# Optimization experiments

Measured on AMD Instinct MI355X. Metric: run time of the kernel, lower is better.

The kernel has to match this reference:

```python
import jax, jax.numpy as jnp
import numpy as np

MAX_NUM_LEVELS = 3.5
NUM_LEVELS = 4  # mip levels 0..3 (levels clamped to [0, 2.5])


def affine_grid(matrix, N, H, W):
    # F.affine_grid, align_corners=False. matrix: (N,2,3) -> grid (N,H,W,2) in xy order.
    xs = (jnp.arange(W, dtype=jnp.float32) + 0.5) * (2.0 / W) - 1.0
    ys = (jnp.arange(H, dtype=jnp.float32) + 0.5) * (2.0 / H) - 1.0
    gy, gx = jnp.meshgrid(ys, xs, indexing='ij')
    base = jnp.stack([gx, gy, jnp.ones_like(gx)], axis=-1)  # (H,W,3)
    return jnp.einsum('hwk,nik->nhwi', base, matrix)  # (N,H,W,2)


def grid_sample_border(img, grid):
    # bilinear grid_sample, padding_mode='border', align_corners=False
    N, C, H, W = img.shape
    x = (grid[..., 0] + 1.0) * (W / 2.0) - 0.5
    y = (grid[..., 1] + 1.0) * (H / 2.0) - 0.5
    x0 = jnp.floor(x); y0 = jnp.floor(y)
    tx = x - x0; ty = y - y0
    x0i = jnp.clip(x0.astype(jnp.int32), 0, W - 1)
    x1i = jnp.clip(x0.astype(jnp.int32) + 1, 0, W - 1)
    y0i = jnp.clip(y0.astype(jnp.int32), 0, H - 1)
    y1i = jnp.clip(y0.astype(jnp.int32) + 1, 0, H - 1)
    b = jnp.arange(N)[:, None, None]
    g = lambda yi, xi: img[b, :, yi, xi]  # (N,Ho,Wo,C) gather
    out = (g(y0i, x0i) * ((1 - tx) * (1 - ty))[..., None]
           + g(y0i, x1i) * (tx * (1 - ty))[..., None]
           + g(y1i, x0i) * ((1 - tx) * ty)[..., None]
           + g(y1i, x1i) * (tx * ty)[..., None])
    return jnp.transpose(out, (0, 3, 1, 2))  # (N,C,Ho,Wo)


def blur_downsample(x):
    N, C, H, W = x.shape
    k1 = jnp.array([1., 3., 3., 1.], dtype=x.dtype) / 8.0
    k = k1[:, None] * k1[None, :]
    xp = jnp.pad(x, ((0, 0), (0, 0), (1, 2), (1, 2)), mode='reflect')
    kernel = jnp.broadcast_to(k[None, None], (C, 1, 4, 4))
    return jax.lax.conv_general_dilated(xp, kernel, window_strides=(2, 2), padding='VALID',
                                        feature_group_count=C,
                                        dimension_numbers=('NCHW', 'OIHW', 'NCHW'))


def compute_levels(grid, H, W):
    # per-pixel mip LOD from local stretch of the sampling grid (in source pixel units)
    coords = (grid + 1.0) * 0.5 * jnp.array([W, H], dtype=grid.dtype)  # (N,Ho,Wo,2)
    dx = coords[:, :-1, 1:] - coords[:, :-1, :-1]
    dy = coords[:, 1:, :-1] - coords[:, :-1, :-1]
    scale = jnp.maximum(jnp.linalg.norm(dx, axis=-1), jnp.linalg.norm(dy, axis=-1))
    scale = jnp.pad(scale, ((0, 0), (0, 1), (0, 1)), mode='edge')  # (N,Ho,Wo)
    levels = jnp.log2(jnp.maximum(scale, 1.0))
    return jnp.clip(levels, 0.0, MAX_NUM_LEVELS - 1.0)


def mipmap_warp(img, grid):
    N, C, H, W = img.shape
    levels = compute_levels(grid, H, W)  # (N,Ho,Wo)
    pyr = [img]
    for _ in range(NUM_LEVELS - 1):
        pyr.append(blur_downsample(pyr[-1]))
    samples = jnp.stack([grid_sample_border(p, grid) for p in pyr], axis=0)  # (L,N,C,Ho,Wo)
    ls = jnp.arange(NUM_LEVELS, dtype=levels.dtype)[:, None, None, None]
    w = jnp.clip(1.0 - jnp.abs(levels[None] - ls), 0.0, 1.0)  # trilinear blend weights (L,N,Ho,Wo)
    return jnp.einsum('lnhw,lnchw->nchw', w, samples)


def setup_inputs() -> dict:
    key = jax.random.key(0)
    k1, k2, k3 = jax.random.split(key, 3)
    N, C, H, W, D = 64, 3, 256, 256, 512
    img = jax.random.normal(k1, (N, C, H, W), dtype=jnp.float32)
    features = jax.random.normal(k2, (N, D), dtype=jnp.float32)
    # learned head params (zero-init in torch; small random here so the warp is nontrivial)
    lin_w = jax.random.normal(k3, (4, D), dtype=jnp.float32) * 0.02
    lin_b = jnp.zeros((4,), dtype=jnp.float32)
    return {'img': img, 'features': features, 'lin_w': lin_w, 'lin_b': lin_b}


def reference(img, features, lin_w, lin_b):
    params = features @ lin_w.T + lin_b  # (N,4)
    rot = jnp.tanh(params[:, 0:1]) * jnp.pi
    scale = jnp.exp(params[:, 1:2])
    sx, sy = params[:, 2:3], params[:, 3:4]
    c, s = jnp.cos(rot), jnp.sin(rot)
    matrix = jnp.concatenate([scale * c, -scale * s, sx, scale * s, scale * c, sy], axis=1).reshape(-1, 2, 3)
    affine_params = jnp.concatenate([rot, scale, sx, sy], axis=1)
    N, C, H, W = img.shape
    grid = affine_grid(matrix, N, H, W)
    out = mipmap_warp(img, grid)
    return out, grid, matrix, affine_params
```

## Files before the change

kernel.cpp:

```cpp
#include <hip/hip_runtime.h>
#include <math.h>

#define N_B 64
#define C_CH 3
#define H_IMG 256
#define W_IMG 256
#define D_FEAT 512

#define OUT_OFF_GRID   12582912
#define OUT_OFF_MATRIX 20971520
#define OUT_OFF_AFFINE 20971904

__global__ void params_kernel(const float* __restrict__ features,
                              const float* __restrict__ lin_w,
                              const float* __restrict__ lin_b,
                              float* __restrict__ out_matrix,
                              float* __restrict__ out_affine,
                              float* __restrict__ ws_params)
{
    const int n = blockIdx.x;
    const int t = threadIdx.x;
    const float* f = features + n * D_FEAT;
    float f0 = f[t];
    float f1 = f[t + 256];
    float a0 = f0 * lin_w[0 * D_FEAT + t] + f1 * lin_w[0 * D_FEAT + t + 256];
    float a1 = f0 * lin_w[1 * D_FEAT + t] + f1 * lin_w[1 * D_FEAT + t + 256];
    float a2 = f0 * lin_w[2 * D_FEAT + t] + f1 * lin_w[2 * D_FEAT + t + 256];
    float a3 = f0 * lin_w[3 * D_FEAT + t] + f1 * lin_w[3 * D_FEAT + t + 256];

    __shared__ float red[4][256];
    red[0][t] = a0; red[1][t] = a1; red[2][t] = a2; red[3][t] = a3;
    __syncthreads();
    for (int s = 128; s > 0; s >>= 1) {
        if (t < s) {
            red[0][t] += red[0][t + s];
            red[1][t] += red[1][t + s];
            red[2][t] += red[2][t + s];
            red[3][t] += red[3][t + s];
        }
        __syncthreads();
    }
    if (t == 0) {
        float p0 = red[0][0] + lin_b[0];
        float p1 = red[1][0] + lin_b[1];
        float p2 = red[2][0] + lin_b[2];
        float p3 = red[3][0] + lin_b[3];
        float rot   = tanhf(p0) * 3.14159265358979323846f;
        float scale = expf(p1);
        float c = cosf(rot), s = sinf(rot);
        float m00 = scale * c, m01 = -scale * s, m02 = p2;
        float m10 = scale * s, m11 =  scale * c, m12 = p3;
        out_matrix[n * 6 + 0] = m00;
        out_matrix[n * 6 + 1] = m01;
        out_matrix[n * 6 + 2] = m02;
        out_matrix[n * 6 + 3] = m10;
        out_matrix[n * 6 + 4] = m11;
        out_matrix[n * 6 + 5] = m12;
        out_affine[n * 4 + 0] = rot;
        out_affine[n * 4 + 1] = scale;
        out_affine[n * 4 + 2] = p2;
        out_affine[n * 4 + 3] = p3;
        float lv = log2f(fmaxf(scale, 1.0f));
        lv = fminf(fmaxf(lv, 0.0f), 2.5f);
        ws_params[n * 8 + 0] = m00;
        ws_params[n * 8 + 1] = m01;
        ws_params[n * 8 + 2] = m02;
        ws_params[n * 8 + 3] = m10;
        ws_params[n * 8 + 4] = m11;
        ws_params[n * 8 + 5] = m12;
        ws_params[n * 8 + 6] = lv;
        ws_params[n * 8 + 7] = 0.0f;
    }
}

template<int Hs, int Ws>
__global__ void down_kernel(const float* __restrict__ src, float* __restrict__ dst)
{
    constexpr int Hd = Hs / 2, Wd = Ws / 2;
    constexpr int PAIRS = Wd / 2;

    const int idx = blockIdx.x * blockDim.x + threadIdx.x;
    const int t   = idx & (PAIRS - 1);
    const int i   = (idx / PAIRS) & (Hd - 1);
    const int nc  = idx / (PAIRS * Hd);

    const float* __restrict__ s = src + (size_t)nc * Hs * Ws;

    int r[4];
#pragma unroll
    for (int a = 0; a < 4; a++) {
        int q = 2 * i + a - 1;
        if (q < 0) q = -q;
        if (q >= Hs) q = 2 * Hs - 2 - q;
        r[a] = q;
    }
    const int c4 = 4 * t;
    const int li = (t > 0)         ? c4 - 1 : 1;
    const int ri = (t < PAIRS - 1) ? c4 + 4 : Ws - 2;

    const float k0 = 0.125f, k1 = 0.375f;
    const float kr[4] = {0.125f, 0.375f, 0.375f, 0.125f};

    float acc0 = 0.0f, acc1 = 0.0f;
#pragma unroll
    for (int a = 0; a < 4; a++) {
        const float* row = s + (size_t)r[a] * Ws;
        float4 v = *(const float4*)(row + c4);
        float L = row[li];
        float R = row[ri];
        float h0 = k0 * L   + k1 * v.x + k1 * v.y + k0 * v.z;
        float h1 = k0 * v.y + k1 * v.z + k1 * v.w + k0 * R;
        acc0 += kr[a] * h0;
        acc1 += kr[a] * h1;
    }
    float2* d2 = (float2*)(dst + (size_t)nc * Hd * Wd + (size_t)i * Wd);
    d2[t] = make_float2(acc0, acc1);
}

__device__ __forceinline__ void sample_level(const float* __restrict__ p, int n, int l,
                                             float X, float Y, float out[3])
{
    const int Wl = W_IMG >> l;
    const int Hl = H_IMG >> l;
    float x = (X + 1.0f) * (0.5f * (float)Wl) - 0.5f;
    float y = (Y + 1.0f) * (0.5f * (float)Hl) - 0.5f;
    float x0f = floorf(x), y0f = floorf(y);
    float tx = x - x0f, ty = y - y0f;
    int x0 = (int)x0f, y0 = (int)y0f;
    int x0i = min(max(x0,     0), Wl - 1);
    int x1i = min(max(x0 + 1, 0), Wl - 1);
    int y0i = min(max(y0,     0), Hl - 1);
    int y1i = min(max(y0 + 1, 0), Hl - 1);
    float w00 = (1.0f - tx) * (1.0f - ty);
    float w01 = tx * (1.0f - ty);
    float w10 = (1.0f - tx) * ty;
    float w11 = tx * ty;
    const float* base = p + (size_t)n * C_CH * Hl * Wl;
#pragma unroll
    for (int c = 0; c < C_CH; c++) {
        const float* pc = base + (size_t)c * Hl * Wl;
        out[c] = w00 * pc[y0i * Wl + x0i] + w01 * pc[y0i * Wl + x1i]
               + w10 * pc[y1i * Wl + x0i] + w11 * pc[y1i * Wl + x1i];
    }
}

__device__ __forceinline__ const float* lvl_ptr(int l, const float* img,
                                                const float* p1, const float* p2,
                                                const float* p3)
{
    return (l == 0) ? img : ((l == 1) ? p1 : ((l == 2) ? p2 : p3));
}

__global__ void warp_kernel(const float* __restrict__ img,
                            const float* __restrict__ pyr1,
                            const float* __restrict__ pyr2,
                            const float* __restrict__ pyr3,
                            const float* __restrict__ ws_params,
                            float* __restrict__ out,
                            float* __restrict__ gridOut)
{
    const int n = blockIdx.y;
    const int tile = blockIdx.x;
    const int w = ((tile & 7) << 5) + (threadIdx.x & 31);
    const int h = ((tile >> 3) << 3) + (threadIdx.x >> 5);

    const float* P = ws_params + n * 8;
    float m00 = P[0], m01 = P[1], m02 = P[2];
    float m10 = P[3], m11 = P[4], m12 = P[5];
    float lv  = P[6];

    float gx = ((float)w + 0.5f) * (2.0f / (float)W_IMG) - 1.0f;
    float gy = ((float)h + 0.5f) * (2.0f / (float)H_IMG) - 1.0f;
    float X = m00 * gx + m01 * gy + m02;
    float Y = m10 * gx + m11 * gy + m12;

    float2* g2 = (float2*)gridOut;
    g2[(size_t)(n * H_IMG + h) * W_IMG + w] = make_float2(X, Y);

    int   l0   = (int)lv;
    float frac = lv - (float)l0;

    float c0[3];
    sample_level(lvl_ptr(l0, img, pyr1, pyr2, pyr3), n, l0, X, Y, c0);

    float r0, r1, r2;
    if (frac > 0.0f) {
        float c1[3];
        sample_level(lvl_ptr(l0 + 1, img, pyr1, pyr2, pyr3), n, l0 + 1, X, Y, c1);
        float w0 = 1.0f - frac;
        r0 = w0 * c0[0] + frac * c1[0];
        r1 = w0 * c0[1] + frac * c1[1];
        r2 = w0 * c0[2] + frac * c1[2];
    } else {
        r0 = c0[0]; r1 = c0[1]; r2 = c0[2];
    }

    size_t base = ((size_t)(n * C_CH + 0) * H_IMG + h) * W_IMG + w;
    out[base]                             = r0;
    out[base + (size_t)H_IMG * W_IMG]     = r1;
    out[base + (size_t)2 * H_IMG * W_IMG] = r2;
}

extern "C" void kernel_launch(void* const* d_in, const int* in_sizes, int n_in,
                              void* d_out, int out_size, void* d_ws, size_t ws_size,
                              hipStream_t stream)
{
    const float* img      = (const float*)d_in[0];
    const float* features = (const float*)d_in[1];
    const float* lin_w    = (const float*)d_in[2];
    const float* lin_b    = (const float*)d_in[3];

    float* out        = (float*)d_out;
    float* gridOut    = out + OUT_OFF_GRID;
    float* out_matrix = out + OUT_OFF_MATRIX;
    float* out_affine = out + OUT_OFF_AFFINE;

    float* ws        = (float*)d_ws;
    float* ws_params = ws;
    float* pyr1 = ws + 1024;
    float* pyr2 = pyr1 + (size_t)N_B * C_CH * 128 * 128;
    float* pyr3 = pyr2 + (size_t)N_B * C_CH * 64 * 64;

    params_kernel<<<N_B, 256, 0, stream>>>(features, lin_w, lin_b,
                                           out_matrix, out_affine, ws_params);

    int t1 = N_B * C_CH * 128 * 64;
    down_kernel<256, 256><<<t1 / 256, 256, 0, stream>>>(img,  pyr1);
    int t2 = N_B * C_CH * 64 * 32;
    down_kernel<128, 128><<<t2 / 256, 256, 0, stream>>>(pyr1, pyr2);
    int t3 = N_B * C_CH * 32 * 16;
    down_kernel<64, 64><<<t3 / 256, 256, 0, stream>>>(pyr2, pyr3);

    warp_kernel<<<dim3(H_IMG * W_IMG / 256, N_B), 256, 0, stream>>>(
        img, pyr1, pyr2, pyr3, ws_params, out, gridOut);
}
```

Before: 198.4 us.

## Widen downsample per-thread output, pair bilinear loads, retile warp, nontemporal stores

The downsample kernel now produces four outputs per thread from two float4 loads, which halves the thread count and widens its stores. Bilinear sampling fetches each horizontal texel pair with a single float2 load, using selects to handle the clamped edges. The warp kernel remaps threads to 16x4 sub-tiles for better 2D gather locality, and writes grid and output with nontemporal stores. The float2 loads may be misaligned when xp is odd, and the new tiling makes the output stores less contiguous.

```diff
diff --git a/kernel.cpp b/kernel.cpp
--- a/kernel.cpp
+++ b/kernel.cpp
@@ -77,12 +77,12 @@
 __global__ void down_kernel(const float* __restrict__ src, float* __restrict__ dst)
 {
     constexpr int Hd = Hs / 2, Wd = Ws / 2;
-    constexpr int PAIRS = Wd / 2;
+    constexpr int QUADS = Wd / 4;
 
     const int idx = blockIdx.x * blockDim.x + threadIdx.x;
-    const int t   = idx & (PAIRS - 1);
-    const int i   = (idx / PAIRS) & (Hd - 1);
-    const int nc  = idx / (PAIRS * Hd);
+    const int t   = idx & (QUADS - 1);
+    const int i   = (idx / QUADS) & (Hd - 1);
+    const int nc  = idx / (QUADS * Hd);
 
     const float* __restrict__ s = src + (size_t)nc * Hs * Ws;
 
@@ -94,31 +94,43 @@
         if (q >= Hs) q = 2 * Hs - 2 - q;
         r[a] = q;
     }
-    const int c4 = 4 * t;
-    const int li = (t > 0)         ? c4 - 1 : 1;
-    const int ri = (t < PAIRS - 1) ? c4 + 4 : Ws - 2;
+    const int c8 = 8 * t;
+    const int li = (t > 0)         ? c8 - 1 : 1;
+    const int ri = (t < QUADS - 1) ? c8 + 8 : Ws - 2;
 
     const float k0 = 0.125f, k1 = 0.375f;
     const float kr[4] = {0.125f, 0.375f, 0.375f, 0.125f};
 
-    float acc0 = 0.0f, acc1 = 0.0f;
+    float acc0 = 0.f, acc1 = 0.f, acc2 = 0.f, acc3 = 0.f;
 #pragma unroll
     for (int a = 0; a < 4; a++) {
         const float* row = s + (size_t)r[a] * Ws;
-        float4 v = *(const float4*)(row + c4);
+        float4 A = *(const float4*)(row + c8);
+        float4 B = *(const float4*)(row + c8 + 4);
         float L = row[li];
         float R = row[ri];
-        float h0 = k0 * L   + k1 * v.x + k1 * v.y + k0 * v.z;
-        float h1 = k0 * v.y + k1 * v.z + k1 * v.w + k0 * R;
+        float h0 = k0 * L   + k1 * A.x + k1 * A.y + k0 * A.z;
+        float h1 = k0 * A.y + k1 * A.z + k1 * A.w + k0 * B.x;
+        float h2 = k0 * A.w + k1 * B.x + k1 * B.y + k0 * B.z;
+        float h3 = k0 * B.y + k1 * B.z + k1 * B.w + k0 * R;
         acc0 += kr[a] * h0;
         acc1 += kr[a] * h1;
-    }
-    float2* d2 = (float2*)(dst + (size_t)nc * Hd * Wd + (size_t)i * Wd);
-    d2[t] = make_float2(acc0, acc1);
-}
-
-__device__ __forceinline__ void sample_level(const float* __restrict__ p, int n, int l,
-                                             float X, float Y, float out[3])
+        acc2 += kr[a] * h2;
+        acc3 += kr[a] * h3;
+    }
+    float4* d4 = (float4*)(dst + (size_t)nc * Hd * Wd + (size_t)i * Wd + 4 * t);
+    *d4 = make_float4(acc0, acc1, acc2, acc3);
+}
+
+__device__ __forceinline__ const float* lvl_ptr(int l, const float* img,
+                                                const float* p1, const float* p2,
+                                                const float* p3)
+{
+    return (l == 0) ? img : ((l == 1) ? p1 : ((l == 2) ? p2 : p3));
+}
+
+__device__ __forceinline__ void sample_level_pair(const float* __restrict__ p, int n, int l,
+                                                  float X, float Y, float out[3])
 {
     const int Wl = W_IMG >> l;
     const int Hl = H_IMG >> l;
@@ -127,10 +139,11 @@
     float x0f = floorf(x), y0f = floorf(y);
     float tx = x - x0f, ty = y - y0f;
     int x0 = (int)x0f, y0 = (int)y0f;
-    int x0i = min(max(x0,     0), Wl - 1);
-    int x1i = min(max(x0 + 1, 0), Wl - 1);
     int y0i = min(max(y0,     0), Hl - 1);
     int y1i = min(max(y0 + 1, 0), Hl - 1);
+    int xp = min(max(x0, 0), Wl - 2);
+    const bool selHi0 = (x0 >= Wl - 1);
+    const bool selLo1 = (x0 < 0);
     float w00 = (1.0f - tx) * (1.0f - ty);
     float w01 = tx * (1.0f - ty);
     float w10 = (1.0f - tx) * ty;
@@ -139,16 +152,14 @@
 #pragma unroll
     for (int c = 0; c < C_CH; c++) {
         const float* pc = base + (size_t)c * Hl * Wl;
-        out[c] = w00 * pc[y0i * Wl + x0i] + w01 * pc[y0i * Wl + x1i]
-               + w10 * pc[y1i * Wl + x0i] + w11 * pc[y1i * Wl + x1i];
-    }
-}
-
-__device__ __forceinline__ const float* lvl_ptr(int l, const float* img,
-                                                const float* p1, const float* p2,
-                                                const float* p3)
-{
-    return (l == 0) ? img : ((l == 1) ? p1 : ((l == 2) ? p2 : p3));
+        float2 a = *(const float2*)(pc + y0i * Wl + xp);
+        float2 b = *(const float2*)(pc + y1i * Wl + xp);
+        float t00 = selHi0 ? a.y : a.x;
+        float t01 = selLo1 ? a.x : a.y;
+        float t10 = selHi0 ? b.y : b.x;
+        float t11 = selLo1 ? b.x : b.y;
+        out[c] = w00 * t00 + w01 * t01 + w10 * t10 + w11 * t11;
+    }
 }
 
 __global__ void warp_kernel(const float* __restrict__ img,
@@ -161,8 +172,11 @@
 {
     const int n = blockIdx.y;
     const int tile = blockIdx.x;
-    const int w = ((tile & 7) << 5) + (threadIdx.x & 31);
-    const int h = ((tile >> 3) << 3) + (threadIdx.x >> 5);
+    const int tid = threadIdx.x;
+    const int w0 = (tile & 7) << 5;
+    const int h0 = (tile >> 3) << 3;
+    const int w = w0 + (((tid >> 6) & 1) << 4) + (tid & 15);
+    const int h = h0 + ((tid >> 7) << 2) + ((tid >> 4) & 3);
 
     const float* P = ws_params + n * 8;
     float m00 = P[0], m01 = P[1], m02 = P[2];
@@ -174,31 +188,32 @@
     float X = m00 * gx + m01 * gy + m02;
     float Y = m10 * gx + m11 * gy + m12;
 
-    float2* g2 = (float2*)gridOut;
-    g2[(size_t)(n * H_IMG + h) * W_IMG + w] = make_float2(X, Y);
+    float2* g2 = (float2*)gridOut + ((size_t)(n * H_IMG + h) * W_IMG + w);
+    __builtin_nontemporal_store(X, &g2->x);
+    __builtin_nontemporal_store(Y, &g2->y);
 
     int   l0   = (int)lv;
     float frac = lv - (float)l0;
 
     float c0[3];
-    sample_level(lvl_ptr(l0, img, pyr1, pyr2, pyr3), n, l0, X, Y, c0);
+    sample_level_pair(lvl_ptr(l0, img, pyr1, pyr2, pyr3), n, l0, X, Y, c0);
 
     float r0, r1, r2;
     if (frac > 0.0f) {
         float c1[3];
-        sample_level(lvl_ptr(l0 + 1, img, pyr1, pyr2, pyr3), n, l0 + 1, X, Y, c1);
-        float w0 = 1.0f - frac;
-        r0 = w0 * c0[0] + frac * c1[0];
-        r1 = w0 * c0[1] + frac * c1[1];
-        r2 = w0 * c0[2] + frac * c1[2];
+        sample_level_pair(lvl_ptr(l0 + 1, img, pyr1, pyr2, pyr3), n, l0 + 1, X, Y, c1);
+        float wA = 1.0f - frac;
+        r0 = wA * c0[0] + frac * c1[0];
+        r1 = wA * c0[1] + frac * c1[1];
+        r2 = wA * c0[2] + frac * c1[2];
     } else {
         r0 = c0[0]; r1 = c0[1]; r2 = c0[2];
     }
 
-    size_t base = ((size_t)(n * C_CH + 0) * H_IMG + h) * W_IMG + w;
-    out[base]                             = r0;
-    out[base + (size_t)H_IMG * W_IMG]     = r1;
-    out[base + (size_t)2 * H_IMG * W_IMG] = r2;
+    size_t base = ((size_t)n * C_CH * H_IMG + h) * W_IMG + w;
+    __builtin_nontemporal_store(r0, out + base);
+    __builtin_nontemporal_store(r1, out + base + (size_t)H_IMG * W_IMG);
+    __builtin_nontemporal_store(r2, out + base + (size_t)2 * H_IMG * W_IMG);
 }
 
 extern "C" void kernel_launch(void* const* d_in, const int* in_sizes, int n_in,
@@ -224,11 +239,11 @@
     params_kernel<<<N_B, 256, 0, stream>>>(features, lin_w, lin_b,
                                            out_matrix, out_affine, ws_params);
 
-    int t1 = N_B * C_CH * 128 * 64;
+    int t1 = N_B * C_CH * 128 * 32;
     down_kernel<256, 256><<<t1 / 256, 256, 0, stream>>>(img,  pyr1);
-    int t2 = N_B * C_CH * 64 * 32;
+    int t2 = N_B * C_CH * 64 * 16;
     down_kernel<128, 128><<<t2 / 256, 256, 0, stream>>>(pyr1, pyr2);
-    int t3 = N_B * C_CH * 32 * 16;
+    int t3 = N_B * C_CH * 32 * 8;
     down_kernel<64, 64><<<t3 / 256, 256, 0, stream>>>(pyr2, pyr3);
 
     warp_kernel<<<dim3(H_IMG * W_IMG / 256, N_B), 256, 0, stream>>>(
```

After: 174.6 us. 1.14x faster.
